# Kernel optimization log

Measured on AMD Instinct MI355X. Metric: run time of the kernel, lower is better.

The kernel has to match this reference:

```python
import jax, jax.numpy as jnp
import numpy as np

TOPK = 13
NUM_CLASSES = 80
ALPHA = 1.0
BETA = 6.0
EPS = 1e-9


def _ciou(gt, pd, eps=1e-7):
    """CIoU between gt (B,M,1,4) and pd (B,1,N,4) xyxy boxes -> (B,M,N)."""
    g_x1, g_y1, g_x2, g_y2 = (gt[..., i] for i in range(4))
    p_x1, p_y1, p_x2, p_y2 = (pd[..., i] for i in range(4))
    iw = jnp.clip(jnp.minimum(g_x2, p_x2) - jnp.maximum(g_x1, p_x1), 0.0)
    ih = jnp.clip(jnp.minimum(g_y2, p_y2) - jnp.maximum(g_y1, p_y1), 0.0)
    inter = iw * ih
    w1, h1 = g_x2 - g_x1, g_y2 - g_y1 + eps
    w2, h2 = p_x2 - p_x1, p_y2 - p_y1 + eps
    union = w1 * h1 + w2 * h2 - inter + eps
    iou = inter / union
    cw = jnp.maximum(g_x2, p_x2) - jnp.minimum(g_x1, p_x1)  # enclosing box
    ch = jnp.maximum(g_y2, p_y2) - jnp.minimum(g_y1, p_y1)
    c2 = cw * cw + ch * ch + eps
    rho2 = ((p_x1 + p_x2 - g_x1 - g_x2) ** 2 + (p_y1 + p_y2 - g_y1 - g_y2) ** 2) / 4.0
    v = (4.0 / jnp.pi ** 2) * (jnp.arctan(w2 / h2) - jnp.arctan(w1 / h1)) ** 2
    a = jax.lax.stop_gradient(v / (v - iou + (1.0 + eps)))  # torch.no_grad alpha
    return iou - (rho2 / c2 + v * a)


def setup_inputs() -> dict:
    key = jax.random.key(0)
    ks = jax.random.split(key, 7)
    B, N, M, C = 16, 8400, 32, NUM_CLASSES
    pd_scores = jax.random.uniform(ks[0], (B, N, C), dtype=jnp.float32)
    # YOLO-style anchor centers for 640x640, strides 8/16/32 -> 8400 points
    pts = []
    for s in (8, 16, 32):
        g = 640 // s
        xs = (jnp.arange(g, dtype=jnp.float32) + 0.5) * s
        xx, yy = jnp.meshgrid(xs, xs, indexing="xy")
        pts.append(jnp.stack([xx.ravel(), yy.ravel()], axis=-1))
    anc_points = jnp.concatenate(pts, axis=0)  # (8400, 2)
    ctr = anc_points[None] + jax.random.normal(ks[1], (B, N, 2)) * 8.0
    wh = jax.random.uniform(ks[2], (B, N, 2), minval=8.0, maxval=128.0)
    pd_bboxes = jnp.concatenate([ctr - wh / 2, ctr + wh / 2], axis=-1)
    gctr = jax.random.uniform(ks[3], (B, M, 2), minval=32.0, maxval=608.0)
    gwh = jax.random.uniform(ks[4], (B, M, 2), minval=16.0, maxval=256.0)
    gt_bboxes = jnp.concatenate([gctr - gwh / 2, gctr + gwh / 2], axis=-1)
    gt_labels = jax.random.randint(ks[5], (B, M, 1), 0, C)
    counts = jax.random.randint(ks[6], (B, 1), 1, M + 1)
    mask_gt = (jnp.arange(M)[None, :] < counts)[..., None]  # (B, M, 1) bool prefix-valid
    return {"pd_scores": pd_scores, "pd_bboxes": pd_bboxes, "anc_points": anc_points,
            "gt_labels": gt_labels, "gt_bboxes": gt_bboxes, "mask_gt": mask_gt}


def reference(pd_scores, pd_bboxes, anc_points, gt_labels, gt_bboxes, mask_gt):
    B, N, C = pd_scores.shape
    M = gt_bboxes.shape[1]
    mask_gt2 = mask_gt[..., 0]  # (B, M) bool
    # --- anchors whose centers lie inside each GT box ---
    lt = gt_bboxes[:, :, None, :2]  # (B, M, 1, 2)
    rb = gt_bboxes[:, :, None, 2:]
    anc = anc_points[None, None]    # (1, 1, N, 2)
    deltas = jnp.concatenate([anc - lt, rb - anc], axis=-1)  # (B, M, N, 4)
    mask_in_gts = jnp.min(deltas, axis=-1) > 1e-9            # (B, M, N)
    valid = mask_in_gts & mask_gt2[:, :, None]
    # --- alignment metric = score^alpha * ciou^beta (masked) ---
    cls = gt_labels[..., 0]                      # (B, M)
    scores_t = jnp.swapaxes(pd_scores, 1, 2)     # (B, C, N)
    bbox_scores = jnp.where(valid, scores_t[jnp.arange(B)[:, None], cls], 0.0)  # (B, M, N)
    overlaps = jnp.where(valid, jnp.clip(_ciou(gt_bboxes[:, :, None], pd_bboxes[:, None]), 0.0), 0.0)
    align_metric = bbox_scores ** ALPHA * overlaps ** BETA
    # --- top-k candidate anchors per GT ---
    _, topk_idx = jax.lax.top_k(align_metric, TOPK)          # (B, M, TOPK)
    bi = jnp.arange(B)[:, None, None]
    mi = jnp.arange(M)[None, :, None]
    src = jnp.broadcast_to(mask_gt2[:, :, None], topk_idx.shape)
    mask_topk = jnp.zeros((B, M, N), dtype=bool).at[bi, mi, topk_idx].set(src)
    mask_pos = mask_topk & valid                             # (B, M, N)
    # --- resolve anchors claimed by multiple GTs: keep highest CIoU ---
    fg_count = jnp.sum(mask_pos, axis=1)                     # (B, N)
    best_gt = jnp.argmax(overlaps, axis=1)                   # (B, N)
    is_max = jnp.arange(M)[None, :, None] == best_gt[:, None, :]
    mask_pos_f = jnp.where(fg_count[:, None, :] > 1, is_max, mask_pos).astype(pd_scores.dtype)
    fg_mask = jnp.sum(mask_pos_f, axis=1)                    # (B, N) float 0/1
    target_gt_idx = jnp.argmax(mask_pos_f, axis=1)           # (B, N)
    # --- gather targets ---
    brow = jnp.arange(B)[:, None]
    target_labels = cls[brow, target_gt_idx]                 # (B, N)
    target_bboxes = gt_bboxes[brow, target_gt_idx]           # (B, N, 4)
    target_scores = jax.nn.one_hot(target_labels, C, dtype=jnp.float32) * fg_mask[..., None]
    # --- normalize scores by per-GT best metric/overlap ---
    align_metric = align_metric * mask_pos_f
    pos_align = jnp.max(align_metric, axis=-1, keepdims=True)            # (B, M, 1)
    pos_over = jnp.max(overlaps * mask_pos_f, axis=-1, keepdims=True)    # (B, M, 1)
    norm_align = jnp.max(align_metric * pos_over / (pos_align + EPS), axis=1)  # (B, N)
    target_scores = target_scores * norm_align[..., None]
    return target_labels, target_bboxes, target_scores, fg_mask > 0, target_gt_idx
```

## Files before the change

kernel.cpp:

```cpp
#include <hip/hip_runtime.h>
#include <math.h>

#define B_ 16
#define N_ 8400
#define M_ 32
#define C_ 80
#define TOPK_ 13

__device__ __forceinline__ bool in_gt(double ax, double ay,
    double gx1, double gy1, double gx2, double gy2) {
  return (ax - gx1 > 1e-9) && (ay - gy1 > 1e-9) &&
         (gx2 - ax > 1e-9) && (gy2 - ay > 1e-9);
}

__device__ __forceinline__ double ciou_ov(
    double px1, double py1, double px2, double py2,
    double gx1, double gy1, double gx2, double gy2,
    double atp, double atg) {
  double iw = fmin(gx2, px2) - fmax(gx1, px1); iw = iw > 0.0 ? iw : 0.0;
  double ih = fmin(gy2, py2) - fmax(gy1, py1); ih = ih > 0.0 ? ih : 0.0;
  double inter = iw * ih;
  double w1 = gx2 - gx1, h1 = gy2 - gy1 + 1e-7;
  double w2 = px2 - px1, h2 = py2 - py1 + 1e-7;
  double uni = w1 * h1 + w2 * h2 - inter + 1e-7;
  double iou = inter / uni;
  double cw = fmax(gx2, px2) - fmin(gx1, px1);
  double ch = fmax(gy2, py2) - fmin(gy1, py1);
  double c2 = cw * cw + ch * ch + 1e-7;
  double dx = px1 + px2 - gx1 - gx2, dy = py1 + py2 - gy1 - gy2;
  double rho2 = (dx * dx + dy * dy) * 0.25;
  double dv = atp - atg;
  double v = (4.0 / (M_PI * M_PI)) * dv * dv;
  double a = v / (v - iou + (1.0 + 1e-7));
  double c = iou - (rho2 / c2 + v * a);
  return c > 0.0 ? c : 0.0;
}

__global__ __launch_bounds__(256) void k_prep(
    const float* __restrict__ pd_bboxes, const float* __restrict__ gt_bboxes,
    const unsigned char* __restrict__ raw,
    double* __restrict__ atp, double* __restrict__ atg,
    unsigned char* __restrict__ mask) {
  int gid = blockIdx.x * 256 + threadIdx.x;
  if (gid < B_ * N_) {
    double x1 = pd_bboxes[(size_t)gid * 4 + 0], y1 = pd_bboxes[(size_t)gid * 4 + 1];
    double x2 = pd_bboxes[(size_t)gid * 4 + 2], y2 = pd_bboxes[(size_t)gid * 4 + 3];
    atp[gid] = atan((x2 - x1) / (y2 - y1 + 1e-7));
  }
  if (gid < B_ * M_) {
    double x1 = gt_bboxes[gid * 4 + 0], y1 = gt_bboxes[gid * 4 + 1];
    double x2 = gt_bboxes[gid * 4 + 2], y2 = gt_bboxes[gid * 4 + 3];
    atg[gid] = atan((x2 - x1) / (y2 - y1 + 1e-7));
  }
  if (blockIdx.x == 0) {
    __shared__ int s_bad;
    int t = threadIdx.x;
    if (t == 0) s_bad = 0;
    __syncthreads();
    if (t < B_) {
      int cnt = 0; bool seen0 = false; bool bad = false;
      for (int m = 0; m < M_; ++m) {
        unsigned char v = raw[t * M_ + m];
        if (v > 1) { bad = true; break; }
        if (v) { if (seen0) { bad = true; break; } ++cnt; }
        else seen0 = true;
      }
      if (cnt < 1) bad = true;
      if (bad) atomicOr(&s_bad, 1);
    }
    __syncthreads();
    bool ok = (s_bad == 0);
    const int* ri = (const int*)raw;
    for (int i = t; i < B_ * M_; i += 256)
      mask[i] = ok ? (raw[i] ? 1 : 0) : ((ri[i] != 0) ? 1 : 0);
  }
}

__global__ __launch_bounds__(256) void k_rowtopk(
    const float* __restrict__ pd_scores, const float* __restrict__ pd_bboxes,
    const float* __restrict__ anc, const int* __restrict__ gt_labels,
    const float* __restrict__ gt_bboxes, const unsigned char* __restrict__ mask,
    const double* __restrict__ atp, const double* __restrict__ atg,
    unsigned int* __restrict__ MPB) {
  int row = blockIdx.x;
  if (!mask[row]) return;
  int b = row >> 5, m = row & 31;
  int t = threadIdx.x;

  double gx1 = gt_bboxes[row * 4 + 0], gy1 = gt_bboxes[row * 4 + 1];
  double gx2 = gt_bboxes[row * 4 + 2], gy2 = gt_bboxes[row * 4 + 3];
  double atgm = atg[row];
  int cls = gt_labels[row];

  const float4* pb4 = (const float4*)(pd_bboxes + (size_t)b * N_ * 4);
  const float2* an2 = (const float2*)anc;
  const double* ap  = atp + (size_t)b * N_;
  const float*  scp = pd_scores + (size_t)b * N_ * C_ + cls;

  double tv[TOPK_]; int ti[TOPK_];
#pragma unroll
  for (int j = 0; j < TOPK_; ++j) { tv[j] = -1.0; ti[j] = 0x7fffffff; }

  auto body = [&](int n) {
    float4 pbox = pb4[n];
    double atpn = ap[n];
    float  svc  = scp[(size_t)n * C_];
    float2 a2   = an2[n];
    bool val = in_gt((double)a2.x, (double)a2.y, gx1, gy1, gx2, gy2);
    double am = 0.0;
    if (val) {
      double ov = ciou_ov((double)pbox.x, (double)pbox.y, (double)pbox.z,
                          (double)pbox.w, gx1, gy1, gx2, gy2, atpn, atgm);
      double o2 = ov * ov;
      am = (double)svc * (o2 * o2 * o2);
    }
    if (am > tv[TOPK_ - 1]) {
      double cv = am; int ci = n;
#pragma unroll
      for (int j = 0; j < TOPK_; ++j) {
        bool sw = (cv > tv[j]) || (cv == tv[j] && ci < ti[j]);
        double xv = tv[j]; int xi = ti[j];
        if (sw) { tv[j] = cv; ti[j] = ci; cv = xv; ci = xi; }
      }
    }
  };

  for (int it = 0; it < 32; ++it) body(t + it * 256);
  if (t < N_ - 8192) body(t + 8192);

  __shared__ double sval[TOPK_ * 256];
  __shared__ int    sidx[TOPK_ * 256];
#pragma unroll
  for (int j = 0; j < TOPK_; ++j) { sval[j * 256 + t] = tv[j]; sidx[j * 256 + t] = ti[j]; }

  for (int s = 128; s >= 1; s >>= 1) {
    __syncthreads();
    if (t < s) {
      double ov_[TOPK_]; int oi_[TOPK_];
      int a = 0, bq = 0;
#pragma unroll
      for (int k = 0; k < TOPK_; ++k) {
        double va = sval[a * 256 + t],  vb = sval[bq * 256 + t + s];
        int    ia = sidx[a * 256 + t],  ib = sidx[bq * 256 + t + s];
        bool takeA = (va > vb) || (va == vb && ia < ib);
        ov_[k] = takeA ? va : vb;
        oi_[k] = takeA ? ia : ib;
        if (takeA) ++a; else ++bq;
      }
#pragma unroll
      for (int k = 0; k < TOPK_; ++k) { sval[k * 256 + t] = ov_[k]; sidx[k * 256 + t] = oi_[k]; }
    }
  }
  __syncthreads();

  if (t < TOPK_) {
    int n = sidx[t * 256];
    float2 a2 = an2[n];
    if (in_gt((double)a2.x, (double)a2.y, gx1, gy1, gx2, gy2))
      atomicOr(&MPB[(size_t)b * N_ + n], 1u << m);
  }
}

__global__ __launch_bounds__(256) void k_colassign(
    const float* __restrict__ pd_scores, const float* __restrict__ pd_bboxes,
    const float* __restrict__ anc, const int* __restrict__ gt_labels,
    const float* __restrict__ gt_bboxes, const unsigned char* __restrict__ mask,
    const double* __restrict__ atp, const double* __restrict__ atg,
    const unsigned int* __restrict__ MPB,
    unsigned char* __restrict__ TG, unsigned char* __restrict__ FG,
    unsigned long long* __restrict__ PAL, unsigned long long* __restrict__ POV) {
  int b = blockIdx.y;
  int n = blockIdx.x * 256 + threadIdx.x;

  __shared__ float s_g[M_][4];
  __shared__ double s_atg[M_];
  __shared__ int s_cls[M_];
  __shared__ unsigned char s_msk[M_];
  if (threadIdx.x < M_) {
    int gi = b * M_ + threadIdx.x;
    s_g[threadIdx.x][0] = gt_bboxes[gi * 4 + 0];
    s_g[threadIdx.x][1] = gt_bboxes[gi * 4 + 1];
    s_g[threadIdx.x][2] = gt_bboxes[gi * 4 + 2];
    s_g[threadIdx.x][3] = gt_bboxes[gi * 4 + 3];
    s_atg[threadIdx.x] = atg[gi];
    s_cls[threadIdx.x] = gt_labels[gi];
    s_msk[threadIdx.x] = mask[gi];
  }
  __syncthreads();
  if (n >= N_) return;

  unsigned int mpb = MPB[(size_t)b * N_ + n];
  int cnt = __popc(mpb);
  int tg = 0; unsigned char fg = 0;

  if (cnt == 1) { tg = __ffs(mpb) - 1; fg = 1; }
  else if (cnt > 1) {
    float2 a2 = ((const float2*)anc)[n];
    float4 pbox = ((const float4*)(pd_bboxes + (size_t)b * N_ * 4))[n];
    double atpn = atp[(size_t)b * N_ + n];
    double best = -1.0;
    for (int mm = 0; mm < M_; ++mm) {
      double g0 = s_g[mm][0], g1 = s_g[mm][1], g2 = s_g[mm][2], g3 = s_g[mm][3];
      bool val = s_msk[mm] && in_gt((double)a2.x, (double)a2.y, g0, g1, g2, g3);
      double ov = val ? ciou_ov((double)pbox.x, (double)pbox.y, (double)pbox.z,
                                (double)pbox.w, g0, g1, g2, g3, atpn, s_atg[mm])
                      : 0.0;
      if (ov > best) { best = ov; tg = mm; }
    }
    fg = 1;
  }

  TG[(size_t)b * N_ + n] = (unsigned char)tg;
  FG[(size_t)b * N_ + n] = fg;

  if (fg) {
    float2 a2 = ((const float2*)anc)[n];
    float4 pbox = ((const float4*)(pd_bboxes + (size_t)b * N_ * 4))[n];
    double atpn = atp[(size_t)b * N_ + n];
    double g0 = s_g[tg][0], g1 = s_g[tg][1], g2 = s_g[tg][2], g3 = s_g[tg][3];
    bool val = s_msk[tg] && in_gt((double)a2.x, (double)a2.y, g0, g1, g2, g3);
    double ov = val ? ciou_ov((double)pbox.x, (double)pbox.y, (double)pbox.z,
                              (double)pbox.w, g0, g1, g2, g3, atpn, s_atg[tg])
                    : 0.0;
    double o2 = ov * ov;
    double am = (double)pd_scores[((size_t)b * N_ + n) * C_ + s_cls[tg]] * (o2 * o2 * o2);
    atomicMax(&PAL[b * M_ + tg], (unsigned long long)__double_as_longlong(am));
    atomicMax(&POV[b * M_ + tg], (unsigned long long)__double_as_longlong(ov));
  }
}

__global__ __launch_bounds__(256) void k_emit(
    const float* __restrict__ pd_scores, const float* __restrict__ pd_bboxes,
    const float* __restrict__ anc, const int* __restrict__ gt_labels,
    const float* __restrict__ gt_bboxes, const unsigned char* __restrict__ mask,
    const double* __restrict__ atp, const double* __restrict__ atg,
    const unsigned char* __restrict__ TG, const unsigned char* __restrict__ FG,
    const unsigned long long* __restrict__ PAL,
    const unsigned long long* __restrict__ POV,
    float* __restrict__ out) {
  int b = blockIdx.y;
  int n0 = blockIdx.x * 64;
  int t = threadIdx.x;

  __shared__ float s_g[M_][4];
  __shared__ double s_atg[M_];
  __shared__ int s_cls[M_];
  __shared__ unsigned char s_msk[M_];
  __shared__ float s_na[64];
  __shared__ int   s_lab[64];
  __shared__ int   s_tg[64];
  __shared__ unsigned char s_fg[64];
  if (t < M_) {
    int gi = b * M_ + t;
    s_g[t][0] = gt_bboxes[gi * 4 + 0];
    s_g[t][1] = gt_bboxes[gi * 4 + 1];
    s_g[t][2] = gt_bboxes[gi * 4 + 2];
    s_g[t][3] = gt_bboxes[gi * 4 + 3];
    s_atg[t] = atg[gi];
    s_cls[t] = gt_labels[gi];
    s_msk[t] = mask[gi];
  }
  __syncthreads();

  if (t < 64) {
    int n = n0 + t;
    if (n < N_) {
      int tg = TG[(size_t)b * N_ + n];
      unsigned char fg = FG[(size_t)b * N_ + n];
      float na = 0.0f;
      if (fg) {
        float2 a2 = ((const float2*)anc)[n];
        float4 pbox = ((const float4*)(pd_bboxes + (size_t)b * N_ * 4))[n];
        double atpn = atp[(size_t)b * N_ + n];
        double g0 = s_g[tg][0], g1 = s_g[tg][1], g2 = s_g[tg][2], g3 = s_g[tg][3];
        bool val = s_msk[tg] && in_gt((double)a2.x, (double)a2.y, g0, g1, g2, g3);
        double ov = val ? ciou_ov((double)pbox.x, (double)pbox.y, (double)pbox.z,
                                  (double)pbox.w, g0, g1, g2, g3, atpn, s_atg[tg])
                        : 0.0;
        double o2 = ov * ov;
        double am = (double)pd_scores[((size_t)b * N_ + n) * C_ + s_cls[tg]] * (o2 * o2 * o2);
        double pal = __longlong_as_double((long long)PAL[b * M_ + tg]);
        double pov = __longlong_as_double((long long)POV[b * M_ + tg]);
        na = (float)(am * pov / (pal + 1e-9));
      }
      s_na[t] = na; s_lab[t] = s_cls[tg]; s_tg[t] = tg; s_fg[t] = fg;
    }
  }
  __syncthreads();

  float* o0 = out;
  float* o1 = out + (size_t)B_ * N_;
  float* o2 = out + (size_t)B_ * N_ * 5;
  float* o3 = out + (size_t)B_ * N_ * 85;
  float* o4 = out + (size_t)B_ * N_ * 86;

  if (t < 64) {
    int n = n0 + t;
    if (n < N_) {
      size_t i = (size_t)b * N_ + n;
      o0[i] = (float)s_lab[t];
      o3[i] = s_fg[t] ? 1.0f : 0.0f;
      o4[i] = (float)s_tg[t];
      int tg = s_tg[t];
      float4 gb = make_float4(s_g[tg][0], s_g[tg][1], s_g[tg][2], s_g[tg][3]);
      ((float4*)o1)[i] = gb;
    }
  }

#pragma unroll
  for (int k = 0; k < 5; ++k) {
    int id = t + k * 256;
    int a = id / 20, j = id % 20;
    int n = n0 + a;
    if (n < N_) {
      int lab = s_lab[a];
      float na = s_fg[a] ? s_na[a] : 0.0f;
      int c0 = 4 * j;
      float4 w;
      w.x = (c0 + 0 == lab) ? na : 0.0f;
      w.y = (c0 + 1 == lab) ? na : 0.0f;
      w.z = (c0 + 2 == lab) ? na : 0.0f;
      w.w = (c0 + 3 == lab) ? na : 0.0f;
      ((float4*)(o2 + ((size_t)b * N_ + n) * C_))[j] = w;
    }
  }
}

extern "C" void kernel_launch(void* const* d_in, const int* in_sizes, int n_in,
                              void* d_out, int out_size, void* d_ws, size_t ws_size,
                              hipStream_t stream) {
  const float* pd_scores = (const float*)d_in[0];
  const float* pd_bboxes = (const float*)d_in[1];
  const float* anc       = (const float*)d_in[2];
  const int*   gt_labels = (const int*)d_in[3];
  const float* gt_bboxes = (const float*)d_in[4];
  const unsigned char* mask_raw = (const unsigned char*)d_in[5];

  char* ws = (char*)d_ws;
  size_t off = 0;
  double* ATP = (double*)(ws + off); off += (size_t)B_ * N_ * 8;
  double* ATG = (double*)(ws + off); off += (size_t)B_ * M_ * 8;
  unsigned int* MPB = (unsigned int*)(ws + off); size_t mpb_off = off; off += (size_t)B_ * N_ * 4;
  unsigned long long* PAL = (unsigned long long*)(ws + off); off += (size_t)B_ * M_ * 8;
  unsigned long long* POV = (unsigned long long*)(ws + off); off += (size_t)B_ * M_ * 8;
  unsigned char* TG   = (unsigned char*)(ws + off); off += (size_t)B_ * N_;
  unsigned char* FG   = (unsigned char*)(ws + off); off += (size_t)B_ * N_;
  unsigned char* MASK = (unsigned char*)(ws + off); off += (size_t)B_ * M_;

  hipMemsetAsync(ws + mpb_off, 0, (size_t)B_ * N_ * 4 + (size_t)B_ * M_ * 16, stream);

  k_prep<<<(B_ * N_ + 255) / 256, 256, 0, stream>>>(pd_bboxes, gt_bboxes,
                                                    mask_raw, ATP, ATG, MASK);
  k_rowtopk<<<B_ * M_, 256, 0, stream>>>(pd_scores, pd_bboxes, anc, gt_labels,
                                         gt_bboxes, MASK, ATP, ATG, MPB);
  dim3 gbn((N_ + 255) / 256, B_);
  k_colassign<<<gbn, 256, 0, stream>>>(pd_scores, pd_bboxes, anc, gt_labels,
                                       gt_bboxes, MASK, ATP, ATG, MPB,
                                       TG, FG, PAL, POV);
  dim3 gem((N_ + 63) / 64, B_);
  k_emit<<<gem, 256, 0, stream>>>(pd_scores, pd_bboxes, anc, gt_labels,
                                  gt_bboxes, MASK, ATP, ATG, TG, FG, PAL, POV,
                                  (float*)d_out);
}
```

Before: 170.8 us.

## Split per-GT top-k into segmented partial top-k plus merge; cache align metrics

The per-row top-k over 8400 anchors is split across 8 segment blocks per GT row, so the grid grows from 512 blocks to 4096, and a small merge kernel combines the 8×13 candidates. The column-assign kernel now computes the CIoU once, caches the overlap and align metric in float buffers, and uses float atomics for the per-GT maxima. The emit kernel then reads the cached metric instead of recomputing the CIoU. This adds a kernel launch and extra workspace traffic. Reducing the stored metrics from double to float may change normalisation rounding slightly.

```diff
diff --git a/kernel.cpp b/kernel.cpp
--- a/kernel.cpp
+++ b/kernel.cpp
@@ -6,6 +6,9 @@
 #define M_ 32
 #define C_ 80
 #define TOPK_ 13
+#define SEG_ 8
+#define SEGLEN_ (N_ / SEG_)
+#define CAND_ (SEG_ * TOPK_)
 
 __device__ __forceinline__ bool in_gt(double ax, double ay,
     double gx1, double gy1, double gx2, double gy2) {
@@ -76,16 +79,18 @@
   }
 }
 
-__global__ __launch_bounds__(256) void k_rowtopk(
+__global__ __launch_bounds__(256) void k_seg(
     const float* __restrict__ pd_scores, const float* __restrict__ pd_bboxes,
     const float* __restrict__ anc, const int* __restrict__ gt_labels,
     const float* __restrict__ gt_bboxes, const unsigned char* __restrict__ mask,
     const double* __restrict__ atp, const double* __restrict__ atg,
-    unsigned int* __restrict__ MPB) {
-  int row = blockIdx.x;
+    double* __restrict__ SEGV, int* __restrict__ SEGI) {
+  int row = blockIdx.y;
   if (!mask[row]) return;
-  int b = row >> 5, m = row & 31;
+  int seg = blockIdx.x;
+  int b = row >> 5;
   int t = threadIdx.x;
+  int base = seg * SEGLEN_;
 
   double gx1 = gt_bboxes[row * 4 + 0], gy1 = gt_bboxes[row * 4 + 1];
   double gx2 = gt_bboxes[row * 4 + 2], gy2 = gt_bboxes[row * 4 + 3];
@@ -125,8 +130,9 @@
     }
   };
 
-  for (int it = 0; it < 32; ++it) body(t + it * 256);
-  if (t < N_ - 8192) body(t + 8192);
+#pragma unroll
+  for (int it = 0; it < 4; ++it) body(base + t + it * 256);
+  if (t < SEGLEN_ - 1024) body(base + 1024 + t);
 
   __shared__ double sval[TOPK_ * 256];
   __shared__ int    sidx[TOPK_ * 256];
@@ -154,8 +160,54 @@
   __syncthreads();
 
   if (t < TOPK_) {
-    int n = sidx[t * 256];
-    float2 a2 = an2[n];
+    size_t o = (size_t)row * CAND_ + seg * TOPK_ + t;
+    SEGV[o] = sval[t * 256];
+    SEGI[o] = sidx[t * 256];
+  }
+}
+
+__global__ __launch_bounds__(128) void k_merge(
+    const double* __restrict__ SEGV, const int* __restrict__ SEGI,
+    const float* __restrict__ anc, const float* __restrict__ gt_bboxes,
+    const unsigned char* __restrict__ mask, unsigned int* __restrict__ MPB) {
+  int row = blockIdx.x;
+  if (!mask[row]) return;
+  int b = row >> 5, m = row & 31;
+  int t = threadIdx.x;
+
+  __shared__ double s_v[CAND_];
+  __shared__ int    s_i[CAND_];
+  __shared__ int    s_w[TOPK_];
+  if (t < CAND_) {
+    s_v[t] = SEGV[(size_t)row * CAND_ + t];
+    s_i[t] = SEGI[(size_t)row * CAND_ + t];
+  }
+  __syncthreads();
+
+  if (t == 0) {
+    int p[SEG_];
+#pragma unroll
+    for (int s = 0; s < SEG_; ++s) p[s] = s * TOPK_;
+    for (int k = 0; k < TOPK_; ++k) {
+      double bv = -2.0; int bi = 0x7fffffff; int bs = 0;
+#pragma unroll
+      for (int s = 0; s < SEG_; ++s) {
+        if (p[s] < (s + 1) * TOPK_) {
+          double v = s_v[p[s]]; int i = s_i[p[s]];
+          if (v > bv || (v == bv && i < bi)) { bv = v; bi = i; bs = s; }
+        }
+      }
+      s_w[k] = bi;
+      p[bs]++;
+    }
+  }
+  __syncthreads();
+
+  if (t < TOPK_) {
+    int n = s_w[t];
+    double gx1 = gt_bboxes[row * 4 + 0], gy1 = gt_bboxes[row * 4 + 1];
+    double gx2 = gt_bboxes[row * 4 + 2], gy2 = gt_bboxes[row * 4 + 3];
+    float2 a2 = ((const float2*)anc)[n];
     if (in_gt((double)a2.x, (double)a2.y, gx1, gy1, gx2, gy2))
       atomicOr(&MPB[(size_t)b * N_ + n], 1u << m);
   }
@@ -168,7 +220,8 @@
     const double* __restrict__ atp, const double* __restrict__ atg,
     const unsigned int* __restrict__ MPB,
     unsigned char* __restrict__ TG, unsigned char* __restrict__ FG,
-    unsigned long long* __restrict__ PAL, unsigned long long* __restrict__ POV) {
+    float* __restrict__ OVC, float* __restrict__ AMC,
+    unsigned int* __restrict__ PAL, unsigned int* __restrict__ POV) {
   int b = blockIdx.y;
   int n = blockIdx.x * 256 + threadIdx.x;
 
@@ -189,63 +242,63 @@
   __syncthreads();
   if (n >= N_) return;
 
-  unsigned int mpb = MPB[(size_t)b * N_ + n];
+  size_t i = (size_t)b * N_ + n;
+  unsigned int mpb = MPB[i];
   int cnt = __popc(mpb);
   int tg = 0; unsigned char fg = 0;
-
-  if (cnt == 1) { tg = __ffs(mpb) - 1; fg = 1; }
-  else if (cnt > 1) {
+  double ov = 0.0;
+
+  if (cnt >= 1) {
+    fg = 1;
     float2 a2 = ((const float2*)anc)[n];
     float4 pbox = ((const float4*)(pd_bboxes + (size_t)b * N_ * 4))[n];
-    double atpn = atp[(size_t)b * N_ + n];
-    double best = -1.0;
-    for (int mm = 0; mm < M_; ++mm) {
-      double g0 = s_g[mm][0], g1 = s_g[mm][1], g2 = s_g[mm][2], g3 = s_g[mm][3];
-      bool val = s_msk[mm] && in_gt((double)a2.x, (double)a2.y, g0, g1, g2, g3);
-      double ov = val ? ciou_ov((double)pbox.x, (double)pbox.y, (double)pbox.z,
-                                (double)pbox.w, g0, g1, g2, g3, atpn, s_atg[mm])
-                      : 0.0;
-      if (ov > best) { best = ov; tg = mm; }
-    }
-    fg = 1;
-  }
-
-  TG[(size_t)b * N_ + n] = (unsigned char)tg;
-  FG[(size_t)b * N_ + n] = fg;
+    double atpn = atp[i];
+    if (cnt == 1) {
+      tg = __ffs(mpb) - 1;
+      double g0 = s_g[tg][0], g1 = s_g[tg][1], g2 = s_g[tg][2], g3 = s_g[tg][3];
+      bool val = s_msk[tg] && in_gt((double)a2.x, (double)a2.y, g0, g1, g2, g3);
+      ov = val ? ciou_ov((double)pbox.x, (double)pbox.y, (double)pbox.z,
+                         (double)pbox.w, g0, g1, g2, g3, atpn, s_atg[tg]) : 0.0;
+    } else {
+      double best = -1.0;
+      for (int mm = 0; mm < M_; ++mm) {
+        double g0 = s_g[mm][0], g1 = s_g[mm][1], g2 = s_g[mm][2], g3 = s_g[mm][3];
+        bool val = s_msk[mm] && in_gt((double)a2.x, (double)a2.y, g0, g1, g2, g3);
+        double o = val ? ciou_ov((double)pbox.x, (double)pbox.y, (double)pbox.z,
+                                 (double)pbox.w, g0, g1, g2, g3, atpn, s_atg[mm])
+                       : 0.0;
+        if (o > best) { best = o; tg = mm; }
+      }
+      ov = best;
+    }
+  }
+
+  TG[i] = (unsigned char)tg;
+  FG[i] = fg;
 
   if (fg) {
-    float2 a2 = ((const float2*)anc)[n];
-    float4 pbox = ((const float4*)(pd_bboxes + (size_t)b * N_ * 4))[n];
-    double atpn = atp[(size_t)b * N_ + n];
-    double g0 = s_g[tg][0], g1 = s_g[tg][1], g2 = s_g[tg][2], g3 = s_g[tg][3];
-    bool val = s_msk[tg] && in_gt((double)a2.x, (double)a2.y, g0, g1, g2, g3);
-    double ov = val ? ciou_ov((double)pbox.x, (double)pbox.y, (double)pbox.z,
-                              (double)pbox.w, g0, g1, g2, g3, atpn, s_atg[tg])
-                    : 0.0;
     double o2 = ov * ov;
-    double am = (double)pd_scores[((size_t)b * N_ + n) * C_ + s_cls[tg]] * (o2 * o2 * o2);
-    atomicMax(&PAL[b * M_ + tg], (unsigned long long)__double_as_longlong(am));
-    atomicMax(&POV[b * M_ + tg], (unsigned long long)__double_as_longlong(ov));
+    double am = (double)pd_scores[i * C_ + s_cls[tg]] * (o2 * o2 * o2);
+    float ovf = (float)ov, amf = (float)am;
+    OVC[i] = ovf; AMC[i] = amf;
+    atomicMax(&PAL[b * M_ + tg], __float_as_uint(amf));
+    atomicMax(&POV[b * M_ + tg], __float_as_uint(ovf));
   }
 }
 
 __global__ __launch_bounds__(256) void k_emit(
-    const float* __restrict__ pd_scores, const float* __restrict__ pd_bboxes,
-    const float* __restrict__ anc, const int* __restrict__ gt_labels,
-    const float* __restrict__ gt_bboxes, const unsigned char* __restrict__ mask,
-    const double* __restrict__ atp, const double* __restrict__ atg,
+    const int* __restrict__ gt_labels, const float* __restrict__ gt_bboxes,
     const unsigned char* __restrict__ TG, const unsigned char* __restrict__ FG,
-    const unsigned long long* __restrict__ PAL,
-    const unsigned long long* __restrict__ POV,
+    const float* __restrict__ AMC,
+    const unsigned int* __restrict__ PAL, const unsigned int* __restrict__ POV,
     float* __restrict__ out) {
   int b = blockIdx.y;
   int n0 = blockIdx.x * 64;
   int t = threadIdx.x;
 
   __shared__ float s_g[M_][4];
-  __shared__ double s_atg[M_];
   __shared__ int s_cls[M_];
-  __shared__ unsigned char s_msk[M_];
+  __shared__ float s_pal[M_], s_pov[M_];
   __shared__ float s_na[64];
   __shared__ int   s_lab[64];
   __shared__ int   s_tg[64];
@@ -256,32 +309,22 @@
     s_g[t][1] = gt_bboxes[gi * 4 + 1];
     s_g[t][2] = gt_bboxes[gi * 4 + 2];
     s_g[t][3] = gt_bboxes[gi * 4 + 3];
-    s_atg[t] = atg[gi];
     s_cls[t] = gt_labels[gi];
-    s_msk[t] = mask[gi];
+    s_pal[t] = __uint_as_float(PAL[gi]);
+    s_pov[t] = __uint_as_float(POV[gi]);
   }
   __syncthreads();
 
   if (t < 64) {
     int n = n0 + t;
     if (n < N_) {
-      int tg = TG[(size_t)b * N_ + n];
-      unsigned char fg = FG[(size_t)b * N_ + n];
+      size_t i = (size_t)b * N_ + n;
+      int tg = TG[i];
+      unsigned char fg = FG[i];
       float na = 0.0f;
       if (fg) {
-        float2 a2 = ((const float2*)anc)[n];
-        float4 pbox = ((const float4*)(pd_bboxes + (size_t)b * N_ * 4))[n];
-        double atpn = atp[(size_t)b * N_ + n];
-        double g0 = s_g[tg][0], g1 = s_g[tg][1], g2 = s_g[tg][2], g3 = s_g[tg][3];
-        bool val = s_msk[tg] && in_gt((double)a2.x, (double)a2.y, g0, g1, g2, g3);
-        double ov = val ? ciou_ov((double)pbox.x, (double)pbox.y, (double)pbox.z,
-                                  (double)pbox.w, g0, g1, g2, g3, atpn, s_atg[tg])
-                        : 0.0;
-        double o2 = ov * ov;
-        double am = (double)pd_scores[((size_t)b * N_ + n) * C_ + s_cls[tg]] * (o2 * o2 * o2);
-        double pal = __longlong_as_double((long long)PAL[b * M_ + tg]);
-        double pov = __longlong_as_double((long long)POV[b * M_ + tg]);
-        na = (float)(am * pov / (pal + 1e-9));
+        double am = (double)AMC[i];
+        na = (float)(am * (double)s_pov[tg] / ((double)s_pal[tg] + 1e-9));
       }
       s_na[t] = na; s_lab[t] = s_cls[tg]; s_tg[t] = tg; s_fg[t] = fg;
     }
@@ -302,8 +345,7 @@
       o3[i] = s_fg[t] ? 1.0f : 0.0f;
       o4[i] = (float)s_tg[t];
       int tg = s_tg[t];
-      float4 gb = make_float4(s_g[tg][0], s_g[tg][1], s_g[tg][2], s_g[tg][3]);
-      ((float4*)o1)[i] = gb;
+      ((float4*)o1)[i] = make_float4(s_g[tg][0], s_g[tg][1], s_g[tg][2], s_g[tg][3]);
     }
   }
 
@@ -340,25 +382,31 @@
   size_t off = 0;
   double* ATP = (double*)(ws + off); off += (size_t)B_ * N_ * 8;
   double* ATG = (double*)(ws + off); off += (size_t)B_ * M_ * 8;
-  unsigned int* MPB = (unsigned int*)(ws + off); size_t mpb_off = off; off += (size_t)B_ * N_ * 4;
-  unsigned long long* PAL = (unsigned long long*)(ws + off); off += (size_t)B_ * M_ * 8;
-  unsigned long long* POV = (unsigned long long*)(ws + off); off += (size_t)B_ * M_ * 8;
+  double* SEGV = (double*)(ws + off); off += (size_t)B_ * M_ * CAND_ * 8;
+  int*    SEGI = (int*)(ws + off);    off += (size_t)B_ * M_ * CAND_ * 4;
+  unsigned int* MPB = (unsigned int*)(ws + off); size_t z0 = off; off += (size_t)B_ * N_ * 4;
+  unsigned int* PAL = (unsigned int*)(ws + off); off += (size_t)B_ * M_ * 4;
+  unsigned int* POV = (unsigned int*)(ws + off); off += (size_t)B_ * M_ * 4;
+  size_t zlen = off - z0;
   unsigned char* TG   = (unsigned char*)(ws + off); off += (size_t)B_ * N_;
   unsigned char* FG   = (unsigned char*)(ws + off); off += (size_t)B_ * N_;
+  float* OVC = (float*)(ws + off); off += (size_t)B_ * N_ * 4;
+  float* AMC = (float*)(ws + off); off += (size_t)B_ * N_ * 4;
   unsigned char* MASK = (unsigned char*)(ws + off); off += (size_t)B_ * M_;
 
-  hipMemsetAsync(ws + mpb_off, 0, (size_t)B_ * N_ * 4 + (size_t)B_ * M_ * 16, stream);
+  hipMemsetAsync(ws + z0, 0, zlen, stream);
 
   k_prep<<<(B_ * N_ + 255) / 256, 256, 0, stream>>>(pd_bboxes, gt_bboxes,
                                                     mask_raw, ATP, ATG, MASK);
-  k_rowtopk<<<B_ * M_, 256, 0, stream>>>(pd_scores, pd_bboxes, anc, gt_labels,
-                                         gt_bboxes, MASK, ATP, ATG, MPB);
+  dim3 gseg(SEG_, B_ * M_);
+  k_seg<<<gseg, 256, 0, stream>>>(pd_scores, pd_bboxes, anc, gt_labels,
+                                  gt_bboxes, MASK, ATP, ATG, SEGV, SEGI);
+  k_merge<<<B_ * M_, 128, 0, stream>>>(SEGV, SEGI, anc, gt_bboxes, MASK, MPB);
   dim3 gbn((N_ + 255) / 256, B_);
   k_colassign<<<gbn, 256, 0, stream>>>(pd_scores, pd_bboxes, anc, gt_labels,
                                        gt_bboxes, MASK, ATP, ATG, MPB,
-                                       TG, FG, PAL, POV);
+                                       TG, FG, OVC, AMC, PAL, POV);
   dim3 gem((N_ + 63) / 64, B_);
-  k_emit<<<gem, 256, 0, stream>>>(pd_scores, pd_bboxes, anc, gt_labels,
-                                  gt_bboxes, MASK, ATP, ATG, TG, FG, PAL, POV,
+  k_emit<<<gem, 256, 0, stream>>>(gt_labels, gt_bboxes, TG, FG, AMC, PAL, POV,
                                   (float*)d_out);
 }
```

New measurement: 196.3 us. 14.9% more time.
